# Kernel tuning notes

Hardware: AMD Instinct MI355X
Metric: run time of the kernel (lower is better)

Reference implementation:

```python
import jax, jax.numpy as jnp
import numpy as np

N_NODES = 50000
N_EDGES = 800000
D_IN = 128
D_HID = 128
N_CLS = 47


def setup_inputs() -> dict:
    key = jax.random.key(0)
    ks = jax.random.split(key, 10)
    inp = {
        "features": jax.random.normal(ks[0], (N_NODES, D_IN), dtype=jnp.float32),
        "src": jax.random.randint(ks[1], (N_EDGES,), 0, N_NODES),
        "dst": jax.random.randint(ks[2], (N_EDGES,), 0, N_NODES),
        "Wself0": jax.random.normal(ks[3], (D_IN, D_HID), dtype=jnp.float32) / np.sqrt(D_IN),
        "Wneigh0": jax.random.normal(ks[4], (D_IN, D_HID), dtype=jnp.float32) / np.sqrt(D_IN),
        "b0": jnp.zeros((D_HID,), dtype=jnp.float32),
        "Wself1": jax.random.normal(ks[5], (D_HID, D_HID), dtype=jnp.float32) / np.sqrt(D_HID),
        "Wneigh1": jax.random.normal(ks[6], (D_HID, D_HID), dtype=jnp.float32) / np.sqrt(D_HID),
        "b1": jnp.zeros((D_HID,), dtype=jnp.float32),
        "Wself2": jax.random.normal(ks[7], (D_HID, N_CLS), dtype=jnp.float32) / np.sqrt(D_HID),
        "Wneigh2": jax.random.normal(ks[8], (D_HID, N_CLS), dtype=jnp.float32) / np.sqrt(D_HID),
        "b2": jnp.zeros((N_CLS,), dtype=jnp.float32),
    }
    return inp


def reference(features, src, dst, Wself0, Wneigh0, b0, Wself1, Wneigh1, b1, Wself2, Wneigh2, b2):
    # GraphSAGE (DGL SAGEConv, aggregator_type='mean', eval mode so dropout is identity).
    # Per layer: h_neigh[v] = mean_{(u->v) in E} h[u]; out = h @ W_self + h_neigh @ W_neigh + b
    n = features.shape[0]
    # in-degree for mean aggregation (zero-degree nodes get zero neighbor feature)
    deg = jax.ops.segment_sum(jnp.ones(dst.shape, dtype=features.dtype), dst, num_segments=n)
    inv_deg = (1.0 / jnp.maximum(deg, 1.0))[:, None]  # [N,1]

    def sage_layer(h, Ws, Wn, b, act):
        # gather src features per edge, scatter-add into dst, normalize by in-degree
        agg = jax.ops.segment_sum(h[src], dst, num_segments=n) * inv_deg  # [N, d]
        out = h @ Ws + agg @ Wn + b
        return jax.nn.relu(out) if act else out

    h = sage_layer(features, Wself0, Wneigh0, b0, True)
    h = sage_layer(h, Wself1, Wneigh1, b1, True)
    h = sage_layer(h, Wself2, Wneigh2, b2, False)
    return h
```

## Files before the change

kernel.cpp:

```cpp
#include <hip/hip_runtime.h>

#define D 128
#define NCLS 47
#define CAP 64

typedef short short8 __attribute__((ext_vector_type(8)));
typedef float floatx4 __attribute__((ext_vector_type(4)));

__device__ inline float bf16lo(unsigned int u) {
    union { unsigned int i; float f; } c; c.i = u << 16; return c.f;
}
__device__ inline float bf16hi(unsigned int u) {
    union { unsigned int i; float f; } c; c.i = u & 0xffff0000u; return c.f;
}
__device__ inline unsigned short f2bf(float f) {
    union { float f; unsigned int i; } c; c.f = f;
    unsigned int r = c.i + 0x7fffu + ((c.i >> 16) & 1u);
    return (unsigned short)(r >> 16);
}

__global__ void prep_kernel(const float* __restrict__ f, unsigned int* __restrict__ hx,
                            int npairs, int* __restrict__ cnt, int n,
                            const float* __restrict__ Ws0, const float* __restrict__ Wn0,
                            unsigned short* __restrict__ Wt0,
                            const float* __restrict__ Ws1, const float* __restrict__ Wn1,
                            unsigned short* __restrict__ Wt1,
                            const float* __restrict__ Ws2, const float* __restrict__ Wn2,
                            unsigned short* __restrict__ Wt2) {
    int gid = blockIdx.x * blockDim.x + threadIdx.x;
    if (gid < npairs) {
        float2 v = ((const float2*)f)[gid];
        unsigned int u = (unsigned int)f2bf(v.x) | ((unsigned int)f2bf(v.y) << 16);
        hx[(size_t)(gid >> 6) * 128 + (gid & 63)] = u;
        return;
    }
    int r = gid - npairs;
    if (r < n) { cnt[r] = 0; return; }
    r -= n;
    if (r < 128 * 256) {
        int nn = r >> 8, k = r & 255;
        float v = (k < 128) ? Ws0[k * 128 + nn] : Wn0[(k - 128) * 128 + nn];
        Wt0[nn * 256 + k] = f2bf(v);
        return;
    }
    r -= 128 * 256;
    if (r < 128 * 256) {
        int nn = r >> 8, k = r & 255;
        float v = (k < 128) ? Ws1[k * 128 + nn] : Wn1[(k - 128) * 128 + nn];
        Wt1[nn * 256 + k] = f2bf(v);
        return;
    }
    r -= 128 * 256;
    if (r < 48 * 256) {
        int nn = r >> 8, k = r & 255;
        float v = 0.0f;
        if (nn < NCLS) v = (k < 128) ? Ws2[k * NCLS + nn] : Wn2[(k - 128) * NCLS + nn];
        Wt2[nn * 256 + k] = f2bf(v);
    }
}

__global__ void fill_csr_kernel(const int* __restrict__ src, const int* __restrict__ dst,
                                int* __restrict__ cnt, int* __restrict__ csr, int n_edges) {
    int e = blockIdx.x * blockDim.x + threadIdx.x;
    if (e < n_edges) {
        int d = dst[e];
        int pos = atomicAdd(&cnt[d], 1);
        if (pos < CAP) csr[d * CAP + pos] = src[e];
    }
}

__global__ __launch_bounds__(256) void gather_kernel(unsigned int* __restrict__ hx,
                                                     const int* __restrict__ csr,
                                                     const int* __restrict__ cnt, int n) {
    int tid = blockIdx.x * blockDim.x + threadIdx.x;
    int node = tid >> 6;
    int lane = tid & 63;
    if (node >= n) return;
    int d = cnt[node];
    if (d > CAP) d = CAP;
    const int4* crow = (const int4*)(csr + node * CAP);
    float a0x = 0.f, a0y = 0.f, a1x = 0.f, a1y = 0.f;
    float a2x = 0.f, a2y = 0.f, a3x = 0.f, a3y = 0.f;
    int nq = d >> 2;
    for (int q = 0; q < nq; ++q) {
        int4 s = crow[q];
        unsigned int u0 = hx[(size_t)s.x * 128 + lane];
        unsigned int u1 = hx[(size_t)s.y * 128 + lane];
        unsigned int u2 = hx[(size_t)s.z * 128 + lane];
        unsigned int u3 = hx[(size_t)s.w * 128 + lane];
        a0x += bf16lo(u0); a0y += bf16hi(u0);
        a1x += bf16lo(u1); a1y += bf16hi(u1);
        a2x += bf16lo(u2); a2y += bf16hi(u2);
        a3x += bf16lo(u3); a3y += bf16hi(u3);
    }
    for (int e = nq << 2; e < d; ++e) {
        int s = csr[node * CAP + e];
        unsigned int u0 = hx[(size_t)s * 128 + lane];
        a0x += bf16lo(u0); a0y += bf16hi(u0);
    }
    float inv = 1.0f / fmaxf((float)d, 1.0f);
    float rx = ((a0x + a1x) + (a2x + a3x)) * inv;
    float ry = ((a0y + a1y) + (a2y + a3y)) * inv;
    hx[(size_t)node * 128 + 64 + lane] = (unsigned int)f2bf(rx) | ((unsigned int)f2bf(ry) << 16);
}

__global__ __launch_bounds__(256) void mfma_layer_kernel(unsigned int* __restrict__ hx,
                                                         const unsigned short* __restrict__ Wt,
                                                         const float* __restrict__ bias,
                                                         int n, int relu) {
    int wave = threadIdx.x >> 6;
    int lane = threadIdx.x & 63;
    int node_base = blockIdx.x * 64 + wave * 16;
    int m = lane & 15;
    int quad = lane >> 4;
    int row_node = node_base + m;
    if (row_node >= n) row_node = n - 1;
    const unsigned short* hx_s = (const unsigned short*)hx;

    floatx4 acc[8];
#pragma unroll
    for (int t = 0; t < 8; ++t) acc[t] = (floatx4){0.f, 0.f, 0.f, 0.f};

    for (int ko = 0; ko < 256; ko += 32) {
        short8 a = *(const short8*)(hx_s + (size_t)row_node * 256 + ko + quad * 8);
#pragma unroll
        for (int t = 0; t < 8; ++t) {
            short8 bfr = *(const short8*)(Wt + (size_t)(t * 16 + m) * 256 + ko + quad * 8);
            acc[t] = __builtin_amdgcn_mfma_f32_16x16x32_bf16(a, bfr, acc[t], 0, 0, 0);
        }
    }

    unsigned short* hw = (unsigned short*)hx;
#pragma unroll
    for (int t = 0; t < 8; ++t) {
        int nfeat = t * 16 + m;
        float bb = bias[nfeat];
#pragma unroll
        for (int r = 0; r < 4; ++r) {
            int node = node_base + quad * 4 + r;
            if (node < n) {
                float v = acc[t][r] + bb;
                if (relu) v = fmaxf(v, 0.0f);
                hw[(size_t)node * 256 + nfeat] = f2bf(v);
            }
        }
    }
}

__global__ __launch_bounds__(256) void mfma_out_kernel(const unsigned int* __restrict__ hx,
                                                       const unsigned short* __restrict__ Wt,
                                                       const float* __restrict__ bias,
                                                       float* __restrict__ out, int n) {
    int wave = threadIdx.x >> 6;
    int lane = threadIdx.x & 63;
    int node_base = blockIdx.x * 64 + wave * 16;
    int m = lane & 15;
    int quad = lane >> 4;
    int row_node = node_base + m;
    if (row_node >= n) row_node = n - 1;
    const unsigned short* hx_s = (const unsigned short*)hx;

    floatx4 acc[3];
#pragma unroll
    for (int t = 0; t < 3; ++t) acc[t] = (floatx4){0.f, 0.f, 0.f, 0.f};

    for (int ko = 0; ko < 256; ko += 32) {
        short8 a = *(const short8*)(hx_s + (size_t)row_node * 256 + ko + quad * 8);
#pragma unroll
        for (int t = 0; t < 3; ++t) {
            short8 bfr = *(const short8*)(Wt + (size_t)(t * 16 + m) * 256 + ko + quad * 8);
            acc[t] = __builtin_amdgcn_mfma_f32_16x16x32_bf16(a, bfr, acc[t], 0, 0, 0);
        }
    }

#pragma unroll
    for (int t = 0; t < 3; ++t) {
        int nfeat = t * 16 + m;
        float bb = (nfeat < NCLS) ? bias[nfeat] : 0.0f;
#pragma unroll
        for (int r = 0; r < 4; ++r) {
            int node = node_base + quad * 4 + r;
            if (node < n && nfeat < NCLS) {
                out[(size_t)node * NCLS + nfeat] = acc[t][r] + bb;
            }
        }
    }
}

extern "C" void kernel_launch(void* const* d_in, const int* in_sizes, int n_in,
                              void* d_out, int out_size, void* d_ws, size_t ws_size,
                              hipStream_t stream) {
    const float* features = (const float*)d_in[0];
    const int* src = (const int*)d_in[1];
    const int* dst = (const int*)d_in[2];
    const float* Wself0 = (const float*)d_in[3];
    const float* Wneigh0 = (const float*)d_in[4];
    const float* b0 = (const float*)d_in[5];
    const float* Wself1 = (const float*)d_in[6];
    const float* Wneigh1 = (const float*)d_in[7];
    const float* b1 = (const float*)d_in[8];
    const float* Wself2 = (const float*)d_in[9];
    const float* Wneigh2 = (const float*)d_in[10];
    const float* b2 = (const float*)d_in[11];
    float* out = (float*)d_out;

    int n = in_sizes[0] / D;
    int n_edges = in_sizes[1];

    int* cnt = (int*)d_ws;
    int* csr = cnt + 50048;
    unsigned int* hx = (unsigned int*)(csr + (size_t)n * CAP);
    unsigned short* Wt0 = (unsigned short*)(hx + (size_t)n * 128);
    unsigned short* Wt1 = Wt0 + 128 * 256;
    unsigned short* Wt2 = Wt1 + 128 * 256;

    int npairs = n * 64;
    int prep_total = npairs + n + 2 * 128 * 256 + 48 * 256;

    prep_kernel<<<(prep_total + 255) / 256, 256, 0, stream>>>(
        features, hx, npairs, cnt, n,
        Wself0, Wneigh0, Wt0, Wself1, Wneigh1, Wt1, Wself2, Wneigh2, Wt2);

    fill_csr_kernel<<<(n_edges + 255) / 256, 256, 0, stream>>>(src, dst, cnt, csr, n_edges);

    int gather_blocks = (n * 64 + 255) / 256;
    int gemm_blocks = (n + 63) / 64;

    gather_kernel<<<gather_blocks, 256, 0, stream>>>(hx, csr, cnt, n);
    mfma_layer_kernel<<<gemm_blocks, 256, 0, stream>>>(hx, Wt0, b0, n, 1);
    gather_kernel<<<gather_blocks, 256, 0, stream>>>(hx, csr, cnt, n);
    mfma_layer_kernel<<<gemm_blocks, 256, 0, stream>>>(hx, Wt1, b1, n, 1);
    gather_kernel<<<gather_blocks, 256, 0, stream>>>(hx, csr, cnt, n);
    mfma_out_kernel<<<gemm_blocks, 256, 0, stream>>>(hx, Wt2, b2, out, n);
}
```

Before: 345.4 us.

## Split hidden/aggregate buffers, 16-bit CSR, uint4 gather with edge-parallel lanes, fuse fill/prep

Separates node features and neighbor aggregates into distinct ping-pong buffers instead of one interleaved array. CSR indices are stored as 16-bit values and the gather reads 16-byte vectors with four edges processed in parallel per wave, then reduced by cross-lane shuffles. CSR fill and feature/weight conversion are merged into one kernel with grid-stride loops, and count zeroing moves to its own small kernel. The 16-bit index only works because node count fits under 65536, which ties correctness to this input size. A zero padding row serves as the dummy source for lanes past the in-degree.

```diff
diff --git a/kernel.cpp b/kernel.cpp
--- a/kernel.cpp
+++ b/kernel.cpp
@@ -18,96 +18,123 @@
     unsigned int r = c.i + 0x7fffu + ((c.i >> 16) & 1u);
     return (unsigned short)(r >> 16);
 }
-
-__global__ void prep_kernel(const float* __restrict__ f, unsigned int* __restrict__ hx,
-                            int npairs, int* __restrict__ cnt, int n,
-                            const float* __restrict__ Ws0, const float* __restrict__ Wn0,
-                            unsigned short* __restrict__ Wt0,
-                            const float* __restrict__ Ws1, const float* __restrict__ Wn1,
-                            unsigned short* __restrict__ Wt1,
-                            const float* __restrict__ Ws2, const float* __restrict__ Wn2,
-                            unsigned short* __restrict__ Wt2) {
-    int gid = blockIdx.x * blockDim.x + threadIdx.x;
-    if (gid < npairs) {
-        float2 v = ((const float2*)f)[gid];
-        unsigned int u = (unsigned int)f2bf(v.x) | ((unsigned int)f2bf(v.y) << 16);
-        hx[(size_t)(gid >> 6) * 128 + (gid & 63)] = u;
+__device__ inline unsigned int pack2(float x, float y) {
+    return (unsigned int)f2bf(x) | ((unsigned int)f2bf(y) << 16);
+}
+
+__global__ void zero_cnt_kernel(int* __restrict__ cnt, int n) {
+    int i = blockIdx.x * blockDim.x + threadIdx.x;
+    if (i < n) cnt[i] = 0;
+}
+
+#define FB 1024
+#define PB 1024
+__global__ __launch_bounds__(256) void fill_prep_kernel(
+    const int* __restrict__ src, const int* __restrict__ dst,
+    int* __restrict__ cnt, unsigned short* __restrict__ csr, int n_edges,
+    const float* __restrict__ f, unsigned int* __restrict__ hA,
+    unsigned int* __restrict__ hB, int npairs, int n,
+    const float* __restrict__ Ws0, const float* __restrict__ Wn0, unsigned short* __restrict__ Wt0,
+    const float* __restrict__ Ws1, const float* __restrict__ Wn1, unsigned short* __restrict__ Wt1,
+    const float* __restrict__ Ws2, const float* __restrict__ Wn2, unsigned short* __restrict__ Wt2) {
+    if (blockIdx.x < FB) {
+        int tid = blockIdx.x * 256 + threadIdx.x;
+        for (int e = tid; e < n_edges; e += FB * 256) {
+            int d = dst[e];
+            int pos = atomicAdd(&cnt[d], 1);
+            if (pos < CAP) csr[d * CAP + pos] = (unsigned short)src[e];
+        }
         return;
     }
-    int r = gid - npairs;
-    if (r < n) { cnt[r] = 0; return; }
-    r -= n;
-    if (r < 128 * 256) {
-        int nn = r >> 8, k = r & 255;
-        float v = (k < 128) ? Ws0[k * 128 + nn] : Wn0[(k - 128) * 128 + nn];
-        Wt0[nn * 256 + k] = f2bf(v);
-        return;
-    }
-    r -= 128 * 256;
-    if (r < 128 * 256) {
-        int nn = r >> 8, k = r & 255;
-        float v = (k < 128) ? Ws1[k * 128 + nn] : Wn1[(k - 128) * 128 + nn];
-        Wt1[nn * 256 + k] = f2bf(v);
-        return;
-    }
-    r -= 128 * 256;
-    if (r < 48 * 256) {
-        int nn = r >> 8, k = r & 255;
-        float v = 0.0f;
-        if (nn < NCLS) v = (k < 128) ? Ws2[k * NCLS + nn] : Wn2[(k - 128) * NCLS + nn];
-        Wt2[nn * 256 + k] = f2bf(v);
-    }
-}
-
-__global__ void fill_csr_kernel(const int* __restrict__ src, const int* __restrict__ dst,
-                                int* __restrict__ cnt, int* __restrict__ csr, int n_edges) {
-    int e = blockIdx.x * blockDim.x + threadIdx.x;
-    if (e < n_edges) {
-        int d = dst[e];
-        int pos = atomicAdd(&cnt[d], 1);
-        if (pos < CAP) csr[d * CAP + pos] = src[e];
-    }
-}
-
-__global__ __launch_bounds__(256) void gather_kernel(unsigned int* __restrict__ hx,
-                                                     const int* __restrict__ csr,
-                                                     const int* __restrict__ cnt, int n) {
+    int tid = (blockIdx.x - FB) * 256 + threadIdx.x;
+    int total = npairs + 128  + 2 * 128 * 256 + 48 * 256;
+    for (int gid = tid; gid < total; gid += PB * 256) {
+        if (gid < npairs) {
+            float2 v = ((const float2*)f)[gid];
+            hA[gid] = pack2(v.x, v.y);
+            continue;
+        }
+        int r = gid - npairs;
+        if (r < 128) {
+            if (r < 64) hA[(size_t)n * 64 + r] = 0u;
+            else hB[(size_t)n * 64 + (r - 64)] = 0u;
+            continue;
+        }
+        r -= 128;
+        if (r < 128 * 256) {
+            int nn = r >> 8, k = r & 255;
+            float v = (k < 128) ? Ws0[k * 128 + nn] : Wn0[(k - 128) * 128 + nn];
+            Wt0[nn * 256 + k] = f2bf(v);
+            continue;
+        }
+        r -= 128 * 256;
+        if (r < 128 * 256) {
+            int nn = r >> 8, k = r & 255;
+            float v = (k < 128) ? Ws1[k * 128 + nn] : Wn1[(k - 128) * 128 + nn];
+            Wt1[nn * 256 + k] = f2bf(v);
+            continue;
+        }
+        r -= 128 * 256;
+        if (r < 48 * 256) {
+            int nn = r >> 8, k = r & 255;
+            float v = 0.0f;
+            if (nn < NCLS) v = (k < 128) ? Ws2[k * NCLS + nn] : Wn2[(k - 128) * NCLS + nn];
+            Wt2[nn * 256 + k] = f2bf(v);
+        }
+    }
+}
+
+__global__ __launch_bounds__(256) void gather_kernel(
+    const uint4* __restrict__ hin,
+    const unsigned short* __restrict__ csr,
+    const int* __restrict__ cnt,
+    uint4* __restrict__ agg,
+    int n) {
     int tid = blockIdx.x * blockDim.x + threadIdx.x;
     int node = tid >> 6;
     int lane = tid & 63;
     if (node >= n) return;
     int d = cnt[node];
     if (d > CAP) d = CAP;
-    const int4* crow = (const int4*)(csr + node * CAP);
-    float a0x = 0.f, a0y = 0.f, a1x = 0.f, a1y = 0.f;
-    float a2x = 0.f, a2y = 0.f, a3x = 0.f, a3y = 0.f;
-    int nq = d >> 2;
-    for (int q = 0; q < nq; ++q) {
-        int4 s = crow[q];
-        unsigned int u0 = hx[(size_t)s.x * 128 + lane];
-        unsigned int u1 = hx[(size_t)s.y * 128 + lane];
-        unsigned int u2 = hx[(size_t)s.z * 128 + lane];
-        unsigned int u3 = hx[(size_t)s.w * 128 + lane];
-        a0x += bf16lo(u0); a0y += bf16hi(u0);
-        a1x += bf16lo(u1); a1y += bf16hi(u1);
-        a2x += bf16lo(u2); a2y += bf16hi(u2);
-        a3x += bf16lo(u3); a3y += bf16hi(u3);
-    }
-    for (int e = nq << 2; e < d; ++e) {
-        int s = csr[node * CAP + e];
-        unsigned int u0 = hx[(size_t)s * 128 + lane];
-        a0x += bf16lo(u0); a0y += bf16hi(u0);
-    }
-    float inv = 1.0f / fmaxf((float)d, 1.0f);
-    float rx = ((a0x + a1x) + (a2x + a3x)) * inv;
-    float ry = ((a0y + a1y) + (a2y + a3y)) * inv;
-    hx[(size_t)node * 128 + 64 + lane] = (unsigned int)f2bf(rx) | ((unsigned int)f2bf(ry) << 16);
-}
-
-__global__ __launch_bounds__(256) void mfma_layer_kernel(unsigned int* __restrict__ hx,
-                                                         const unsigned short* __restrict__ Wt,
-                                                         const float* __restrict__ bias,
-                                                         int n, int relu) {
+    int g = lane >> 4;
+    int c = lane & 15;
+    const unsigned short* crow = csr + node * CAP;
+    float a0 = 0.f, a1 = 0.f, a2 = 0.f, a3 = 0.f, a4 = 0.f, a5 = 0.f, a6 = 0.f, a7 = 0.f;
+    for (int e0 = 0; e0 < d; e0 += 4) {
+        int e = e0 + g;
+        int s = (e < d) ? (int)crow[e] : n;
+        uint4 u = hin[(size_t)s * 16 + c];
+        a0 += bf16lo(u.x); a1 += bf16hi(u.x);
+        a2 += bf16lo(u.y); a3 += bf16hi(u.y);
+        a4 += bf16lo(u.z); a5 += bf16hi(u.z);
+        a6 += bf16lo(u.w); a7 += bf16hi(u.w);
+    }
+    a0 += __shfl_xor(a0, 16); a1 += __shfl_xor(a1, 16);
+    a2 += __shfl_xor(a2, 16); a3 += __shfl_xor(a3, 16);
+    a4 += __shfl_xor(a4, 16); a5 += __shfl_xor(a5, 16);
+    a6 += __shfl_xor(a6, 16); a7 += __shfl_xor(a7, 16);
+    a0 += __shfl_xor(a0, 32); a1 += __shfl_xor(a1, 32);
+    a2 += __shfl_xor(a2, 32); a3 += __shfl_xor(a3, 32);
+    a4 += __shfl_xor(a4, 32); a5 += __shfl_xor(a5, 32);
+    a6 += __shfl_xor(a6, 32); a7 += __shfl_xor(a7, 32);
+    if (g == 0) {
+        float inv = 1.0f / fmaxf((float)d, 1.0f);
+        uint4 o;
+        o.x = pack2(a0 * inv, a1 * inv);
+        o.y = pack2(a2 * inv, a3 * inv);
+        o.z = pack2(a4 * inv, a5 * inv);
+        o.w = pack2(a6 * inv, a7 * inv);
+        agg[(size_t)node * 16 + c] = o;
+    }
+}
+
+__global__ __launch_bounds__(256) void mfma_layer_kernel(
+    const unsigned int* __restrict__ hin,
+    const unsigned int* __restrict__ agg,
+    const unsigned short* __restrict__ Wt,
+    const float* __restrict__ bias,
+    unsigned short* __restrict__ hout,
+    int n) {
     int wave = threadIdx.x >> 6;
     int lane = threadIdx.x & 63;
     int node_base = blockIdx.x * 64 + wave * 16;
@@ -115,22 +142,32 @@
     int quad = lane >> 4;
     int row_node = node_base + m;
     if (row_node >= n) row_node = n - 1;
-    const unsigned short* hx_s = (const unsigned short*)hx;
+    const unsigned short* arow = (const unsigned short*)hin + (size_t)row_node * 128;
+    const unsigned short* grow = (const unsigned short*)agg + (size_t)row_node * 128;
 
     floatx4 acc[8];
 #pragma unroll
     for (int t = 0; t < 8; ++t) acc[t] = (floatx4){0.f, 0.f, 0.f, 0.f};
 
-    for (int ko = 0; ko < 256; ko += 32) {
-        short8 a = *(const short8*)(hx_s + (size_t)row_node * 256 + ko + quad * 8);
+#pragma unroll
+    for (int ko = 0; ko < 128; ko += 32) {
+        short8 a = *(const short8*)(arow + ko + quad * 8);
 #pragma unroll
         for (int t = 0; t < 8; ++t) {
             short8 bfr = *(const short8*)(Wt + (size_t)(t * 16 + m) * 256 + ko + quad * 8);
             acc[t] = __builtin_amdgcn_mfma_f32_16x16x32_bf16(a, bfr, acc[t], 0, 0, 0);
         }
     }
-
-    unsigned short* hw = (unsigned short*)hx;
+#pragma unroll
+    for (int ko = 0; ko < 128; ko += 32) {
+        short8 a = *(const short8*)(grow + ko + quad * 8);
+#pragma unroll
+        for (int t = 0; t < 8; ++t) {
+            short8 bfr = *(const short8*)(Wt + (size_t)(t * 16 + m) * 256 + 128 + ko + quad * 8);
+            acc[t] = __builtin_amdgcn_mfma_f32_16x16x32_bf16(a, bfr, acc[t], 0, 0, 0);
+        }
+    }
+
 #pragma unroll
     for (int t = 0; t < 8; ++t) {
         int nfeat = t * 16 + m;
@@ -139,18 +176,19 @@
         for (int r = 0; r < 4; ++r) {
             int node = node_base + quad * 4 + r;
             if (node < n) {
-                float v = acc[t][r] + bb;
-                if (relu) v = fmaxf(v, 0.0f);
-                hw[(size_t)node * 256 + nfeat] = f2bf(v);
+                float v = fmaxf(acc[t][r] + bb, 0.0f);
+                hout[(size_t)node * 128 + nfeat] = f2bf(v);
             }
         }
     }
 }
 
-__global__ __launch_bounds__(256) void mfma_out_kernel(const unsigned int* __restrict__ hx,
-                                                       const unsigned short* __restrict__ Wt,
-                                                       const float* __restrict__ bias,
-                                                       float* __restrict__ out, int n) {
+__global__ __launch_bounds__(256) void mfma_out_kernel(
+    const unsigned int* __restrict__ hin,
+    const unsigned int* __restrict__ agg,
+    const unsigned short* __restrict__ Wt,
+    const float* __restrict__ bias,
+    float* __restrict__ out, int n) {
     int wave = threadIdx.x >> 6;
     int lane = threadIdx.x & 63;
     int node_base = blockIdx.x * 64 + wave * 16;
@@ -158,30 +196,41 @@
     int quad = lane >> 4;
     int row_node = node_base + m;
     if (row_node >= n) row_node = n - 1;
-    const unsigned short* hx_s = (const unsigned short*)hx;
+    const unsigned short* arow = (const unsigned short*)hin + (size_t)row_node * 128;
+    const unsigned short* grow = (const unsigned short*)agg + (size_t)row_node * 128;
 
     floatx4 acc[3];
 #pragma unroll
     for (int t = 0; t < 3; ++t) acc[t] = (floatx4){0.f, 0.f, 0.f, 0.f};
 
-    for (int ko = 0; ko < 256; ko += 32) {
-        short8 a = *(const short8*)(hx_s + (size_t)row_node * 256 + ko + quad * 8);
+#pragma unroll
+    for (int ko = 0; ko < 128; ko += 32) {
+        short8 a = *(const short8*)(arow + ko + quad * 8);
 #pragma unroll
         for (int t = 0; t < 3; ++t) {
             short8 bfr = *(const short8*)(Wt + (size_t)(t * 16 + m) * 256 + ko + quad * 8);
             acc[t] = __builtin_amdgcn_mfma_f32_16x16x32_bf16(a, bfr, acc[t], 0, 0, 0);
         }
     }
+#pragma unroll
+    for (int ko = 0; ko < 128; ko += 32) {
+        short8 a = *(const short8*)(grow + ko + quad * 8);
+#pragma unroll
+        for (int t = 0; t < 3; ++t) {
+            short8 bfr = *(const short8*)(Wt + (size_t)(t * 16 + m) * 256 + 128 + ko + quad * 8);
+            acc[t] = __builtin_amdgcn_mfma_f32_16x16x32_bf16(a, bfr, acc[t], 0, 0, 0);
+        }
+    }
 
 #pragma unroll
     for (int t = 0; t < 3; ++t) {
         int nfeat = t * 16 + m;
-        float bb = (nfeat < NCLS) ? bias[nfeat] : 0.0f;
-#pragma unroll
-        for (int r = 0; r < 4; ++r) {
-            int node = node_base + quad * 4 + r;
-            if (node < n && nfeat < NCLS) {
-                out[(size_t)node * NCLS + nfeat] = acc[t][r] + bb;
+        if (nfeat < NCLS) {
+            float bb = bias[nfeat];
+#pragma unroll
+            for (int r = 0; r < 4; ++r) {
+                int node = node_base + quad * 4 + r;
+                if (node < n) out[(size_t)node * NCLS + nfeat] = acc[t][r] + bb;
             }
         }
     }
@@ -208,28 +257,29 @@
     int n_edges = in_sizes[1];
 
     int* cnt = (int*)d_ws;
-    int* csr = cnt + 50048;
-    unsigned int* hx = (unsigned int*)(csr + (size_t)n * CAP);
-    unsigned short* Wt0 = (unsigned short*)(hx + (size_t)n * 128);
+    unsigned short* csr = (unsigned short*)(cnt + 50048);
+    unsigned int* hA = (unsigned int*)(csr + (size_t)n * CAP + 32);
+    unsigned int* hB = hA + (size_t)(n + 1) * 64;
+    unsigned int* agg = hB + (size_t)(n + 1) * 64;
+    unsigned short* Wt0 = (unsigned short*)(agg + (size_t)n * 64);
     unsigned short* Wt1 = Wt0 + 128 * 256;
     unsigned short* Wt2 = Wt1 + 128 * 256;
 
     int npairs = n * 64;
-    int prep_total = npairs + n + 2 * 128 * 256 + 48 * 256;
-
-    prep_kernel<<<(prep_total + 255) / 256, 256, 0, stream>>>(
-        features, hx, npairs, cnt, n,
+
+    zero_cnt_kernel<<<(n + 255) / 256, 256, 0, stream>>>(cnt, n);
+    fill_prep_kernel<<<FB + PB, 256, 0, stream>>>(
+        src, dst, cnt, csr, n_edges,
+        features, hA, hB, npairs, n,
         Wself0, Wneigh0, Wt0, Wself1, Wneigh1, Wt1, Wself2, Wneigh2, Wt2);
-
-    fill_csr_kernel<<<(n_edges + 255) / 256, 256, 0, stream>>>(src, dst, cnt, csr, n_edges);
 
     int gather_blocks = (n * 64 + 255) / 256;
     int gemm_blocks = (n + 63) / 64;
 
-    gather_kernel<<<gather_blocks, 256, 0, stream>>>(hx, csr, cnt, n);
-    mfma_layer_kernel<<<gemm_blocks, 256, 0, stream>>>(hx, Wt0, b0, n, 1);
-    gather_kernel<<<gather_blocks, 256, 0, stream>>>(hx, csr, cnt, n);
-    mfma_layer_kernel<<<gemm_blocks, 256, 0, stream>>>(hx, Wt1, b1, n, 1);
-    gather_kernel<<<gather_blocks, 256, 0, stream>>>(hx, csr, cnt, n);
-    mfma_out_kernel<<<gemm_blocks, 256, 0, stream>>>(hx, Wt2, b2, out, n);
-}
+    gather_kernel<<<gather_blocks, 256, 0, stream>>>((const uint4*)hA, csr, cnt, (uint4*)agg, n);
+    mfma_layer_kernel<<<gemm_blocks, 256, 0, stream>>>(hA, agg, Wt0, b0, (unsigned short*)hB, n);
+    gather_kernel<<<gather_blocks, 256, 0, stream>>>((const uint4*)hB, csr, cnt, (uint4*)agg, n);
+    mfma_layer_kernel<<<gemm_blocks, 256, 0, stream>>>(hB, agg, Wt1, b1, (unsigned short*)hA, n);
+    gather_kernel<<<gather_blocks, 256, 0, stream>>>((const uint4*)hA, csr, cnt, (uint4*)agg, n);
+    mfma_out_kernel<<<gemm_blocks, 256, 0, stream>>>(hA, agg, Wt2, b2, out, n);
+}
```

After: 350.0 us. About the same (+1.3%).
